# Performance work log

Hardware: AMD Instinct MI355X
Metric: run time of the kernel (lower is better)

The kernel has to match this reference:

```python
import jax, jax.numpy as jnp
import numpy as np
import math

N_HEAD = 16
N_EMBD = 2048

def setup_inputs() -> dict:
    key = jax.random.key(0)
    k1, k2, k3, k4, k5 = jax.random.split(key, 5)
    B, T, C = 4, 2048, N_EMBD
    x = jax.random.normal(k1, (B, T, C), dtype=jnp.float32)
    # torch Linear stores weight [out,in]; we store [in,out] for x @ W
    s_attn = 1.0 / math.sqrt(C)
    w_attn = jax.random.normal(k2, (C, 3 * C), dtype=jnp.float32) * s_attn
    b_attn = jnp.zeros((3 * C,), dtype=jnp.float32)
    w_proj = jax.random.normal(k3, (C, C), dtype=jnp.float32) * s_attn
    b_proj = jnp.zeros((C,), dtype=jnp.float32)
    return {"x": x, "w_attn": w_attn, "b_attn": b_attn,
            "w_proj": w_proj, "b_proj": b_proj}

def reference(x, w_attn, b_attn, w_proj, b_proj):
    B, T, C = x.shape
    H = N_HEAD
    D = C // H
    qkv = x @ w_attn + b_attn                      # [B,T,3C]
    q, k, v = jnp.split(qkv, 3, axis=2)
    q = q.reshape(B, T, H, D).transpose(0, 2, 1, 3)  # [B,H,T,D]
    k = k.reshape(B, T, H, D).transpose(0, 2, 1, 3)
    v = v.reshape(B, T, H, D).transpose(0, 2, 1, 3)
    scale = 1.0 / math.sqrt(D)
    att = jnp.einsum('bhqd,bhkd->bhqk', q, k) * scale  # [B,H,T,T]
    causal = jnp.tril(jnp.ones((T, T), dtype=bool))    # mask slice bias[:, :, FULL_T-T:FULL_T, :FULL_T] with FULL_T==T
    att = jnp.where(causal[None, None], att, -jnp.inf)
    att = jax.nn.softmax(att.astype(jnp.float32), axis=-1).astype(att.dtype)
    y = jnp.einsum('bhqk,bhkd->bhqd', att, v)          # [B,H,T,D]
    y = y.transpose(0, 2, 1, 3).reshape(B, T, C)
    return y @ w_proj + b_proj
```

## Files before the change

### kernel.cpp

```cpp
#include <hip/hip_runtime.h>
#include <hip/hip_bf16.h>

#define NB 4
#define TT 2048
#define CC 2048
#define HH 16
#define DD 128

typedef short bvec8 __attribute__((ext_vector_type(8)));
typedef float fvec4 __attribute__((ext_vector_type(4)));

__device__ __forceinline__ void gload16(const void* g, void* l) {
  __builtin_amdgcn_global_load_lds(
      (__attribute__((address_space(1))) void*)g,
      (__attribute__((address_space(3))) void*)l, 16, 0, 0);
}

__device__ __forceinline__ unsigned short f2bf(float f) {
  union { float f; unsigned int u; } x; x.f = f;
  unsigned int u = x.u;
  return (unsigned short)((u + 0x7FFFu + ((u >> 16) & 1u)) >> 16);
}

__device__ __forceinline__ fvec4 mfma16(bvec8 a, bvec8 b, fvec4 c) {
  return __builtin_amdgcn_mfma_f32_16x16x32_bf16(a, b, c, 0, 0, 0);
}

#define KSC (0.08838834764831845f * 1.4426950408889634f)

__global__ __launch_bounds__(256) void k_prep(const float* __restrict__ x,
                                              unsigned short* __restrict__ xb,
                                              const float* __restrict__ wa,
                                              unsigned short* __restrict__ wat,
                                              const float* __restrict__ wp,
                                              unsigned short* __restrict__ wpt) {
  __shared__ unsigned short tile[64][65];
  int bid = blockIdx.x;
  int t = threadIdx.x;
  if (bid < 16384) {
    int i = bid * 256 + t;
    float4 v = ((const float4*)x)[i];
    ushort4 o;
    o.x = f2bf(v.x); o.y = f2bf(v.y); o.z = f2bf(v.z); o.w = f2bf(v.w);
    ((ushort4*)xb)[i] = o;
    return;
  }
  const float* in; unsigned short* out; int R, Cn, bx, by;
  int b2 = bid - 16384;
  if (b2 < 3072) {
    in = wa; out = wat; R = 2048; Cn = 6144; bx = b2 % 96; by = b2 / 96;
  } else {
    int b3 = b2 - 3072;
    in = wp; out = wpt; R = 2048; Cn = 2048; bx = b3 % 32; by = b3 / 32;
  }
  int tC = bx * 64, tR = by * 64;
  for (int i = 0; i < 16; i++) {
    int idx = t + i * 256; int r = idx >> 6, c = idx & 63;
    tile[r][c] = f2bf(in[(size_t)(tR + r) * Cn + tC + c]);
  }
  __syncthreads();
  for (int i = 0; i < 16; i++) {
    int idx = t + i * 256; int r = idx >> 6, c = idx & 63;
    out[(size_t)(tC + r) * R + tR + c] = tile[c][r];
  }
}

template <int EPI>
__global__ __launch_bounds__(512, 2) void k_gemm8(
    const unsigned short* __restrict__ A,
    const unsigned short* __restrict__ Bt,
    const float* __restrict__ bias,
    unsigned short* __restrict__ qk,
    unsigned short* __restrict__ vt,
    float* __restrict__ out) {
  const int K = CC;
  const int nt = K / 64;
  __shared__ unsigned short sm[2][32768];

  int tid = threadIdx.x;
  int wid = tid >> 6, ln = tid & 63, gl = ln >> 4, lo = ln & 15;
  int wr = wid >> 2, wc = wid & 3;

  unsigned gx = gridDim.x, gy = gridDim.y;
  unsigned orig = blockIdx.y * gx + blockIdx.x;
  unsigned cpx = (gx * gy) >> 3;
  unsigned wg2 = (orig & 7) * cpx + (orig >> 3);
  int n0 = (int)(wg2 / gy) * 256;
  int m0 = (int)(wg2 % gy) * 256;

  auto stageA = [&](int buf, int half, int kt) {
#pragma unroll
    for (int j = 0; j < 2; j++) {
      int c = j * 512 + tid;
      int r = c >> 3;
      int kc = (c & 7) ^ (r & 7);
      gload16(A + (size_t)(m0 + half * 128 + r) * K + kt * 64 + kc * 8,
              &sm[buf][(size_t)(half * 1024 + c) * 8]);
    }
  };
  auto stageB = [&](int buf, int half, int kt) {
#pragma unroll
    for (int j = 0; j < 2; j++) {
      int c = j * 512 + tid;
      int r = c >> 3;
      int kc = (c & 7) ^ (r & 7);
      gload16(Bt + (size_t)(n0 + half * 128 + r) * K + kt * 64 + kc * 8,
              &sm[buf][16384 + (size_t)(half * 1024 + c) * 8]);
    }
  };

#define AFRAG(buf, mi, ks) \
  (*(const bvec8*)&sm[buf][(((wr * 128 + (mi) * 16 + lo) * 8) + ((((ks) * 4 + gl)) ^ (lo & 7))) * 8])
#define BFRAG(buf, nj, ks) \
  (*(const bvec8*)&sm[buf][16384 + (((wc * 64 + (nj) * 16 + lo) * 8) + ((((ks) * 4 + gl)) ^ (lo & 7))) * 8])

  fvec4 acc[8][4];
  fvec4 zero = {0.f, 0.f, 0.f, 0.f};
#pragma unroll
  for (int i = 0; i < 8; i++)
#pragma unroll
    for (int j = 0; j < 4; j++) acc[i][j] = zero;

  stageA(0, 0, 0); stageA(0, 1, 0); stageB(0, 0, 0); stageB(0, 1, 0);
  stageA(1, 0, 1); stageA(1, 1, 1);

  for (int t = 0; t < nt; t++) {
    int cur = t & 1;
    bvec8 a0[4], a1[4], a2[4], a3[4], b0[4], b1[4];

    if (t + 1 < nt) {
      asm volatile("s_waitcnt vmcnt(4)" ::: "memory");
    } else {
      asm volatile("s_waitcnt vmcnt(0)" ::: "memory");
    }
    __builtin_amdgcn_sched_barrier(0);
    __builtin_amdgcn_s_barrier();
    __builtin_amdgcn_sched_barrier(0);

#pragma unroll
    for (int mi = 0; mi < 4; mi++) a0[mi] = AFRAG(cur, mi, 0);
#pragma unroll
    for (int nj = 0; nj < 4; nj++) b0[nj] = BFRAG(cur, nj, 0);
#pragma unroll
    for (int mi = 0; mi < 4; mi++) a1[mi] = AFRAG(cur, mi + 4, 0);
#pragma unroll
    for (int mi = 0; mi < 4; mi++) a2[mi] = AFRAG(cur, mi, 1);
#pragma unroll
    for (int nj = 0; nj < 4; nj++) b1[nj] = BFRAG(cur, nj, 1);
    if (t + 1 < nt) { stageB(cur ^ 1, 0, t + 1); stageB(cur ^ 1, 1, t + 1); }
    __builtin_amdgcn_sched_barrier(0);

    __builtin_amdgcn_s_setprio(1);
#pragma unroll
    for (int mi = 0; mi < 4; mi++)
#pragma unroll
      for (int nj = 0; nj < 4; nj++) acc[mi][nj] = mfma16(a0[mi], b0[nj], acc[mi][nj]);
    __builtin_amdgcn_s_setprio(0);

#pragma unroll
    for (int mi = 0; mi < 4; mi++) a3[mi] = AFRAG(cur, mi + 4, 1);
    __builtin_amdgcn_sched_barrier(0);

    __builtin_amdgcn_s_setprio(1);
#pragma unroll
    for (int mi = 0; mi < 4; mi++)
#pragma unroll
      for (int nj = 0; nj < 4; nj++) acc[mi + 4][nj] = mfma16(a1[mi], b0[nj], acc[mi + 4][nj]);
    __builtin_amdgcn_s_setprio(0);

    __builtin_amdgcn_s_setprio(1);
#pragma unroll
    for (int mi = 0; mi < 4; mi++)
#pragma unroll
      for (int nj = 0; nj < 4; nj++) acc[mi][nj] = mfma16(a2[mi], b1[nj], acc[mi][nj]);
    __builtin_amdgcn_s_setprio(0);

    asm volatile("s_waitcnt lgkmcnt(0)" ::: "memory");
    __builtin_amdgcn_sched_barrier(0);
    __builtin_amdgcn_s_barrier();
    if (t + 2 < nt) { stageA(cur, 0, t + 2); stageA(cur, 1, t + 2); }

    __builtin_amdgcn_s_setprio(1);
#pragma unroll
    for (int mi = 0; mi < 4; mi++)
#pragma unroll
      for (int nj = 0; nj < 4; nj++) acc[mi + 4][nj] = mfma16(a3[mi], b1[nj], acc[mi + 4][nj]);
    __builtin_amdgcn_s_setprio(0);
  }

  if (EPI == 0) {
    int s = n0 >> 11;
    if (s < 2) {
      unsigned short* se = (unsigned short*)sm;
      float mulv = (s == 1) ? KSC : 1.0f;
#pragma unroll
      for (int nj = 0; nj < 4; nj++) {
        int coln = wc * 64 + nj * 16 + lo;
        float bn = bias[n0 + coln];
#pragma unroll
        for (int mi = 0; mi < 8; mi++) {
          int rowbase = wr * 128 + mi * 16 + gl * 4;
#pragma unroll
          for (int r = 0; r < 4; r++) {
            int row = rowbase + r;
            int colsw = coln ^ (((row >> 2) & 7) << 3);
            se[row * 256 + colsw] = f2bf((acc[mi][nj][r] + bn) * mulv);
          }
        }
      }
      __syncthreads();
#pragma unroll
      for (int k = 0; k < 16; k++) {
        int c = k * 512 + tid;
        int row = c >> 5, cpos = c & 31;
        int cposw = cpos ^ ((row >> 2) & 7);
        bvec8 v = *(const bvec8*)&se[row * 256 + cposw * 8];
        int mb = m0 + row;
        int b = mb >> 11, t0 = mb & 2047;
        int col = cpos * 8;
        int hh = ((n0 + col) >> 7) & 15;
        int d = col & 127;
        *(bvec8*)&qk[((((size_t)s * NB + b) * HH + hh) * TT + t0) * DD + d] = v;
      }
    } else {
#pragma unroll
      for (int nj = 0; nj < 4; nj++) {
        int n = n0 + wc * 64 + nj * 16 + lo;
        float bn = bias[n];
        int hh = (n >> 7) & 15, d = n & 127;
#pragma unroll
        for (int mi = 0; mi < 8; mi++) {
          int mb = m0 + wr * 128 + mi * 16 + gl * 4;
          int b = mb >> 11, t0 = mb & 2047;
          size_t base = ((((size_t)b * HH + hh) * (TT / 8) + (t0 >> 3)) * DD + d) * 8 + (t0 & 7);
          ushort4 o;
          o.x = f2bf(acc[mi][nj][0] + bn);
          o.y = f2bf(acc[mi][nj][1] + bn);
          o.z = f2bf(acc[mi][nj][2] + bn);
          o.w = f2bf(acc[mi][nj][3] + bn);
          *(ushort4*)&vt[base] = o;
        }
      }
    }
  } else {
#pragma unroll
    for (int nj = 0; nj < 4; nj++) {
      int n = n0 + wc * 64 + nj * 16 + lo;
      float bn = bias[n];
#pragma unroll
      for (int mi = 0; mi < 8; mi++) {
        int m = m0 + wr * 128 + mi * 16 + gl * 4;
#pragma unroll
        for (int r = 0; r < 4; r++) out[(size_t)(m + r) * CC + n] = acc[mi][nj][r] + bn;
      }
    }
  }
#undef AFRAG
#undef BFRAG
}

__global__ __launch_bounds__(256, 2) void k_attn(
    const unsigned short* __restrict__ qk,
    const unsigned short* __restrict__ vt,
    unsigned short* __restrict__ yb) {
  __shared__ unsigned short Ks[2][8192];
  __shared__ unsigned short Vs[2][8192];
  __shared__ unsigned short Ps[4][2048];
  int tid = threadIdx.x, wid = tid >> 6, ln = tid & 63;
  int gl = ln >> 4, lo = ln & 15;
  int qp = blockIdx.x & 7;
  int bh = blockIdx.x >> 3;
  int b = bh >> 4, h = bh & 15;
  const unsigned short* Q  = qk + (((size_t)b * HH + h) * TT) * DD;
  const unsigned short* Kg = qk + ((((size_t)NB + b) * HH + h) * TT) * DD;
  const unsigned short* Vg = vt + (((size_t)b * HH + h) * (TT / 8)) * DD * 8;
  fvec4 zero = {0.f, 0.f, 0.f, 0.f};

  auto stageK = [&](int buf, int it) {
    int k0 = it * 64;
#pragma unroll
    for (int j = 0; j < 4; j++) {
      int c = j * 256 + tid;
      int r = c >> 4, cc = c & 15;
      gload16(Kg + (size_t)(k0 + r) * DD + ((cc ^ (r & 7)) * 8), &Ks[buf][(j * 256 + wid * 64) * 8]);
    }
  };
  auto stageV = [&](int buf, int it) {
    int k0 = it * 64;
#pragma unroll
    for (int j = 0; j < 4; j++) {
      int c = j * 256 + tid;
      int cc = c >> 7, d = c & 127;
      gload16(Vg + ((size_t)(k0 / 8 + cc) * DD + d) * 8, &Vs[buf][(j * 256 + wid * 64) * 8]);
    }
  };

  auto smax = [&](fvec4 (&sa)[4], float (&mr)[4], float (&lr)[4], fvec4 (&oa)[8],
                  int q0m, int k0, bool domask, int psoff) {
    float p[4][4], mxl[4];
#pragma unroll
    for (int r = 0; r < 4; r++) {
      int qrow = q0m + gl * 4 + r;
      float m = -1e30f;
      if (domask) {
#pragma unroll
        for (int fn = 0; fn < 4; fn++) {
          int kkg = k0 + fn * 16 + lo;
          float v = (kkg <= qrow) ? sa[fn][r] : -1e30f;
          p[fn][r] = v; m = fmaxf(m, v);
        }
      } else {
#pragma unroll
        for (int fn = 0; fn < 4; fn++) {
          float v = sa[fn][r];
          p[fn][r] = v; m = fmaxf(m, v);
        }
      }
      mxl[r] = m;
    }
    bool c = (mxl[0] > mr[0] + 8.f) || (mxl[1] > mr[1] + 8.f) ||
             (mxl[2] > mr[2] + 8.f) || (mxl[3] > mr[3] + 8.f);
    if (__any(c)) {
#pragma unroll
      for (int r = 0; r < 4; r++) {
        float m = mxl[r];
#pragma unroll
        for (int dlt = 1; dlt < 16; dlt <<= 1) m = fmaxf(m, __shfl_xor(m, dlt));
        float mnew = fmaxf(mr[r], m);
        float corr = exp2f(mr[r] - mnew);
        mr[r] = mnew; lr[r] *= corr;
#pragma unroll
        for (int fd = 0; fd < 8; fd++) oa[fd][r] *= corr;
      }
    }
#pragma unroll
    for (int r = 0; r < 4; r++)
#pragma unroll
      for (int fn = 0; fn < 4; fn++) {
        float pv = exp2f(p[fn][r] - mr[r]);
        p[fn][r] = pv; lr[r] += pv;
      }
#pragma unroll
    for (int fn = 0; fn < 4; fn++)
#pragma unroll
      for (int r = 0; r < 4; r++) {
        int qr = gl * 4 + r;
        int kc = fn * 16 + lo;
        Ps[wid][psoff + (qr * 8 + ((kc >> 3) ^ (qr & 7))) * 8 + (kc & 7)] = f2bf(p[fn][r]);
      }
  };

  for (int pass = 0; pass < 2; pass++) {
    int qt = pass ? (15 - qp) : qp;
    int q0w = qt * 128 + wid * 32;

    bvec8 qf0[4], qf1[4];
#pragma unroll
    for (int ks = 0; ks < 4; ks++) {
      qf0[ks] = *(const bvec8*)(Q + (size_t)(q0w + lo) * DD + ks * 32 + gl * 8);
      qf1[ks] = *(const bvec8*)(Q + (size_t)(q0w + 16 + lo) * DD + ks * 32 + gl * 8);
    }

    fvec4 oacc0[8], oacc1[8];
#pragma unroll
    for (int i = 0; i < 8; i++) { oacc0[i] = zero; oacc1[i] = zero; }
    float mr0[4] = {-1e30f, -1e30f, -1e30f, -1e30f};
    float mr1[4] = {-1e30f, -1e30f, -1e30f, -1e30f};
    float lr0[4] = {0.f, 0.f, 0.f, 0.f};
    float lr1[4] = {0.f, 0.f, 0.f, 0.f};

    int ntiles = 2 * qt + 2;
    stageK(0, 0); stageV(0, 0);
    asm volatile("s_waitcnt vmcnt(8)" ::: "memory");
    __builtin_amdgcn_sched_barrier(0);
    __builtin_amdgcn_s_barrier();
    __builtin_amdgcn_sched_barrier(0);

    for (int it = 0; it < ntiles; it++) {
      int cur = it & 1;
      int k0 = it * 64;
      bool more = (it + 1 < ntiles);
      bool active = (k0 <= q0w + 31);
      if (more) { stageK(cur ^ 1, it + 1); stageV(cur ^ 1, it + 1); }

      fvec4 sa0[4], sa1[4];
      if (active) {
        __builtin_amdgcn_s_setprio(1);
#pragma unroll
        for (int fn = 0; fn < 4; fn++) {
          fvec4 s0 = zero, s1 = zero;
#pragma unroll
          for (int ks = 0; ks < 4; ks++) {
            int r = fn * 16 + lo;
            int cd = ks * 4 + gl;
            bvec8 kf = *(const bvec8*)&Ks[cur][(r * 16 + (cd ^ (r & 7))) * 8];
            s0 = mfma16(qf0[ks], kf, s0);
            s1 = mfma16(qf1[ks], kf, s1);
          }
          sa0[fn] = s0; sa1[fn] = s1;
        }
        __builtin_amdgcn_s_setprio(0);

        smax(sa0, mr0, lr0, oacc0, q0w,      k0, (k0 + 63) > q0w,        0);
        smax(sa1, mr1, lr1, oacc1, q0w + 16, k0, (k0 + 63) > (q0w + 16), 1024);
      }

      if (more) {
        asm volatile("s_waitcnt vmcnt(16)" ::: "memory");
      } else {
        asm volatile("s_waitcnt vmcnt(0)" ::: "memory");
      }
      __builtin_amdgcn_sched_barrier(0);
      __builtin_amdgcn_s_barrier();
      __builtin_amdgcn_sched_barrier(0);

      if (active) {
        __builtin_amdgcn_s_setprio(1);
#pragma unroll
        for (int ks2 = 0; ks2 < 2; ks2++) {
          bvec8 pf0 = *(const bvec8*)&Ps[wid][(lo * 8 + ((ks2 * 4 + gl) ^ (lo & 7))) * 8];
          bvec8 pf1 = *(const bvec8*)&Ps[wid][1024 + (lo * 8 + ((ks2 * 4 + gl) ^ (lo & 7))) * 8];
#pragma unroll
          for (int fd = 0; fd < 8; fd++) {
            bvec8 vf = *(const bvec8*)&Vs[cur][((ks2 * 4 + gl) * 128 + fd * 16 + lo) * 8];
            oacc0[fd] = mfma16(pf0, vf, oacc0[fd]);
            oacc1[fd] = mfma16(pf1, vf, oacc1[fd]);
          }
        }
        __builtin_amdgcn_s_setprio(0);
      }

      if (more) {
        asm volatile("s_waitcnt vmcnt(8)" ::: "memory");
      } else {
        asm volatile("s_waitcnt vmcnt(0)" ::: "memory");
      }
      __builtin_amdgcn_sched_barrier(0);
      __builtin_amdgcn_s_barrier();
      __builtin_amdgcn_sched_barrier(0);
    }

#pragma unroll
    for (int r = 0; r < 4; r++) {
      float l0 = lr0[r], l1 = lr1[r];
#pragma unroll
      for (int dlt = 1; dlt < 16; dlt <<= 1) {
        l0 += __shfl_xor(l0, dlt);
        l1 += __shfl_xor(l1, dlt);
      }
      int qrow0 = q0w + gl * 4 + r;
      int qrow1 = q0w + 16 + gl * 4 + r;
      float inv0 = 1.f / l0, inv1 = 1.f / l1;
#pragma unroll
      for (int fd = 0; fd < 8; fd++) {
        int d = fd * 16 + lo;
        yb[((size_t)b * TT + qrow0) * CC + h * DD + d] = f2bf(oacc0[fd][r] * inv0);
        yb[((size_t)b * TT + qrow1) * CC + h * DD + d] = f2bf(oacc1[fd][r] * inv1);
      }
    }
  }
}

extern "C" void kernel_launch(void* const* d_in, const int* in_sizes, int n_in,
                              void* d_out, int out_size, void* d_ws, size_t ws_size,
                              hipStream_t stream) {
  const float* x      = (const float*)d_in[0];
  const float* w_attn = (const float*)d_in[1];
  const float* b_attn = (const float*)d_in[2];
  const float* w_proj = (const float*)d_in[3];
  const float* b_proj = (const float*)d_in[4];
  float* out = (float*)d_out;

  char* ws = (char*)d_ws;
  unsigned short* xb    = (unsigned short*)(ws);
  unsigned short* wab_t = (unsigned short*)(ws + 33554432);
  unsigned short* wpb_t = (unsigned short*)(ws + 58720256);
  unsigned short* qkws  = (unsigned short*)(ws + 67108864);
  unsigned short* vtws  = (unsigned short*)(ws + 134217728);
  unsigned short* ybws  = (unsigned short*)(ws + 167772160);

  hipLaunchKernelGGL(k_prep, dim3(16384 + 3072 + 1024), dim3(256), 0, stream,
                     x, xb, w_attn, wab_t, w_proj, wpb_t);
  hipLaunchKernelGGL((k_gemm8<0>), dim3(24, 32), dim3(512), 0, stream,
                     xb, wab_t, b_attn, qkws, vtws, (float*)nullptr);
  hipLaunchKernelGGL(k_attn, dim3(512), dim3(256), 0, stream, qkws, vtws, ybws);
  hipLaunchKernelGGL((k_gemm8<1>), dim3(8, 32), dim3(512), 0, stream,
                     ybws, wpb_t, b_proj, (unsigned short*)nullptr, (unsigned short*)nullptr, out);
}
```

Measured before the change: 432.5 us.

## Vectorize weight transpose, fuse dual softmax paths, add epilogue sync

The weight-conversion transpose now uses float4 loads and ushort4 stores instead of scalar accesses, which cuts the number of memory instructions. The two per-fragment softmax calls in the attention loop are merged into one interleaved block with a single __any rescale check, giving more independent instructions to overlap. A waitcnt and barrier are added before the QKV GEMM epilogue reuses shared memory, which looks like a correctness fix for a race. Merging the rescale check means both fragments are rescaled when either needs it, and the fused block may raise register pressure.

Result: slower. 441.9 us (+2.2%).

```diff
diff --git a/kernel.cpp b/kernel.cpp
--- a/kernel.cpp
+++ b/kernel.cpp
@@ -54,14 +54,26 @@
     in = wp; out = wpt; R = 2048; Cn = 2048; bx = b3 % 32; by = b3 / 32;
   }
   int tC = bx * 64, tR = by * 64;
-  for (int i = 0; i < 16; i++) {
-    int idx = t + i * 256; int r = idx >> 6, c = idx & 63;
-    tile[r][c] = f2bf(in[(size_t)(tR + r) * Cn + tC + c]);
+  int rw = t >> 4, c4 = (t & 15) * 4;
+#pragma unroll
+  for (int i = 0; i < 4; i++) {
+    int row = rw + i * 16;
+    float4 v = *(const float4*)&in[(size_t)(tR + row) * Cn + tC + c4];
+    tile[row][c4 + 0] = f2bf(v.x);
+    tile[row][c4 + 1] = f2bf(v.y);
+    tile[row][c4 + 2] = f2bf(v.z);
+    tile[row][c4 + 3] = f2bf(v.w);
   }
   __syncthreads();
-  for (int i = 0; i < 16; i++) {
-    int idx = t + i * 256; int r = idx >> 6, c = idx & 63;
-    out[(size_t)(tC + r) * R + tR + c] = tile[c][r];
+#pragma unroll
+  for (int i = 0; i < 4; i++) {
+    int rr = rw + i * 16;
+    ushort4 o;
+    o.x = tile[c4 + 0][rr];
+    o.y = tile[c4 + 1][rr];
+    o.z = tile[c4 + 2][rr];
+    o.w = tile[c4 + 3][rr];
+    *(ushort4*)&out[(size_t)(tC + rr) * R + tR + c4] = o;
   }
 }
 
@@ -191,6 +203,8 @@
   if (EPI == 0) {
     int s = n0 >> 11;
     if (s < 2) {
+      asm volatile("s_waitcnt lgkmcnt(0)" ::: "memory");
+      __syncthreads();
       unsigned short* se = (unsigned short*)sm;
       float mulv = (s == 1) ? KSC : 1.0f;
 #pragma unroll
@@ -295,61 +309,6 @@
     }
   };
 
-  auto smax = [&](fvec4 (&sa)[4], float (&mr)[4], float (&lr)[4], fvec4 (&oa)[8],
-                  int q0m, int k0, bool domask, int psoff) {
-    float p[4][4], mxl[4];
-#pragma unroll
-    for (int r = 0; r < 4; r++) {
-      int qrow = q0m + gl * 4 + r;
-      float m = -1e30f;
-      if (domask) {
-#pragma unroll
-        for (int fn = 0; fn < 4; fn++) {
-          int kkg = k0 + fn * 16 + lo;
-          float v = (kkg <= qrow) ? sa[fn][r] : -1e30f;
-          p[fn][r] = v; m = fmaxf(m, v);
-        }
-      } else {
-#pragma unroll
-        for (int fn = 0; fn < 4; fn++) {
-          float v = sa[fn][r];
-          p[fn][r] = v; m = fmaxf(m, v);
-        }
-      }
-      mxl[r] = m;
-    }
-    bool c = (mxl[0] > mr[0] + 8.f) || (mxl[1] > mr[1] + 8.f) ||
-             (mxl[2] > mr[2] + 8.f) || (mxl[3] > mr[3] + 8.f);
-    if (__any(c)) {
-#pragma unroll
-      for (int r = 0; r < 4; r++) {
-        float m = mxl[r];
-#pragma unroll
-        for (int dlt = 1; dlt < 16; dlt <<= 1) m = fmaxf(m, __shfl_xor(m, dlt));
-        float mnew = fmaxf(mr[r], m);
-        float corr = exp2f(mr[r] - mnew);
-        mr[r] = mnew; lr[r] *= corr;
-#pragma unroll
-        for (int fd = 0; fd < 8; fd++) oa[fd][r] *= corr;
-      }
-    }
-#pragma unroll
-    for (int r = 0; r < 4; r++)
-#pragma unroll
-      for (int fn = 0; fn < 4; fn++) {
-        float pv = exp2f(p[fn][r] - mr[r]);
-        p[fn][r] = pv; lr[r] += pv;
-      }
-#pragma unroll
-    for (int fn = 0; fn < 4; fn++)
-#pragma unroll
-      for (int r = 0; r < 4; r++) {
-        int qr = gl * 4 + r;
-        int kc = fn * 16 + lo;
-        Ps[wid][psoff + (qr * 8 + ((kc >> 3) ^ (qr & 7))) * 8 + (kc & 7)] = f2bf(p[fn][r]);
-      }
-  };
-
   for (int pass = 0; pass < 2; pass++) {
     int qt = pass ? (15 - qp) : qp;
     int q0w = qt * 128 + wid * 32;
@@ -383,8 +342,8 @@
       bool active = (k0 <= q0w + 31);
       if (more) { stageK(cur ^ 1, it + 1); stageV(cur ^ 1, it + 1); }
 
-      fvec4 sa0[4], sa1[4];
       if (active) {
+        fvec4 sa0[4], sa1[4];
         __builtin_amdgcn_s_setprio(1);
 #pragma unroll
         for (int fn = 0; fn < 4; fn++) {
@@ -401,8 +360,62 @@
         }
         __builtin_amdgcn_s_setprio(0);
 
-        smax(sa0, mr0, lr0, oacc0, q0w,      k0, (k0 + 63) > q0w,        0);
-        smax(sa1, mr1, lr1, oacc1, q0w + 16, k0, (k0 + 63) > (q0w + 16), 1024);
+        float p0[4][4], p1[4][4], mx0[4], mx1[4];
+        bool dm0 = (k0 + 63) > q0w;
+        bool dm1 = (k0 + 63) > (q0w + 16);
+#pragma unroll
+        for (int r = 0; r < 4; r++) {
+          float m0v = -1e30f, m1v = -1e30f;
+#pragma unroll
+          for (int fn = 0; fn < 4; fn++) {
+            int kkg = k0 + fn * 16 + lo;
+            float v0 = (!dm0 || kkg <= (q0w + gl * 4 + r)) ? sa0[fn][r] : -1e30f;
+            float v1 = (!dm1 || kkg <= (q0w + 16 + gl * 4 + r)) ? sa1[fn][r] : -1e30f;
+            p0[fn][r] = v0; m0v = fmaxf(m0v, v0);
+            p1[fn][r] = v1; m1v = fmaxf(m1v, v1);
+          }
+          mx0[r] = m0v; mx1[r] = m1v;
+        }
+        bool g = (mx0[0] > mr0[0] + 8.f) || (mx0[1] > mr0[1] + 8.f) ||
+                 (mx0[2] > mr0[2] + 8.f) || (mx0[3] > mr0[3] + 8.f) ||
+                 (mx1[0] > mr1[0] + 8.f) || (mx1[1] > mr1[1] + 8.f) ||
+                 (mx1[2] > mr1[2] + 8.f) || (mx1[3] > mr1[3] + 8.f);
+        if (__any(g)) {
+#pragma unroll
+          for (int r = 0; r < 4; r++) {
+            float m0v = mx0[r], m1v = mx1[r];
+#pragma unroll
+            for (int dlt = 1; dlt < 16; dlt <<= 1) {
+              m0v = fmaxf(m0v, __shfl_xor(m0v, dlt));
+              m1v = fmaxf(m1v, __shfl_xor(m1v, dlt));
+            }
+            float n0v = fmaxf(mr0[r], m0v), n1v = fmaxf(mr1[r], m1v);
+            float c0 = exp2f(mr0[r] - n0v), c1 = exp2f(mr1[r] - n1v);
+            mr0[r] = n0v; mr1[r] = n1v;
+            lr0[r] *= c0; lr1[r] *= c1;
+#pragma unroll
+            for (int fd = 0; fd < 8; fd++) { oacc0[fd][r] *= c0; oacc1[fd][r] *= c1; }
+          }
+        }
+#pragma unroll
+        for (int r = 0; r < 4; r++)
+#pragma unroll
+          for (int fn = 0; fn < 4; fn++) {
+            float pv0 = exp2f(p0[fn][r] - mr0[r]);
+            float pv1 = exp2f(p1[fn][r] - mr1[r]);
+            p0[fn][r] = pv0; lr0[r] += pv0;
+            p1[fn][r] = pv1; lr1[r] += pv1;
+          }
+#pragma unroll
+        for (int fn = 0; fn < 4; fn++)
+#pragma unroll
+          for (int r = 0; r < 4; r++) {
+            int qr = gl * 4 + r;
+            int kc = fn * 16 + lo;
+            int off = (qr * 8 + ((kc >> 3) ^ (qr & 7))) * 8 + (kc & 7);
+            Ps[wid][off] = f2bf(p0[fn][r]);
+            Ps[wid][1024 + off] = f2bf(p1[fn][r]);
+          }
       }
 
       if (more) {
```
